# Performance work log

Measured on AMD Instinct MI355X. Metric: run time of the kernel, lower is better.

The kernel has to match this reference:

```python
import jax, jax.numpy as jnp
import numpy as np

IN_FEATURES = 256
N_HEADS = 4
N_HIDDEN = 128  # out_features, concat=False
SLOPE = 0.1
NEG_INF = -9e15


def setup_inputs() -> dict:
    key = jax.random.key(0)
    k1, k2, k3, k4 = jax.random.split(key, 4)
    N = 8192
    h = jax.random.normal(k1, (N, IN_FEATURES), dtype=jnp.float32)
    adj_mat = jax.random.randint(k2, (N, N), 0, 2, dtype=jnp.int32)
    # xavier_normal with gain=1.414
    std_W = 1.414 * (2.0 / (IN_FEATURES + N_HIDDEN * N_HEADS)) ** 0.5
    W = jax.random.normal(k3, (IN_FEATURES, N_HIDDEN * N_HEADS), dtype=jnp.float32) * std_W
    std_a = 1.414 * (2.0 / (2 * N_HIDDEN + 1)) ** 0.5
    a = jax.random.normal(k4, (N_HEADS, 2 * N_HIDDEN, 1), dtype=jnp.float32) * std_a
    return {"h": h, "adj_mat": adj_mat, "W": W, "a": a}


def reference(h, adj_mat, W, a):
    N = h.shape[0]
    # linear projection -> [H, N, d]
    ht = (h @ W).reshape(N, N_HEADS, N_HIDDEN).transpose(1, 0, 2)
    # dropout is identity (eval / p effectively 0), then LeakyReLU
    ht = jnp.where(ht >= 0, ht, SLOPE * ht)
    # additive attention scores: src[h,i] + tgt[h,j]
    src = jnp.einsum('hnd,hd->hn', ht, a[:, :N_HIDDEN, 0])  # [H, N]
    tgt = jnp.einsum('hnd,hd->hn', ht, a[:, N_HIDDEN:, 0])  # [H, N]
    e = src[:, :, None] + tgt[:, None, :]                   # [H, N, N]
    e = jnp.where(adj_mat[None, :, :] > 0, e, NEG_INF)
    attn = jax.nn.softmax(e, axis=-1)
    # weighted sum and mean over heads (concat=False)
    out = jnp.einsum('hnm,hmd->hnd', attn, ht).mean(axis=0)  # [N, d]
    return out
```

## Files before the change

kernel.cpp:

```cpp
#include <hip/hip_runtime.h>


typedef unsigned short u16;
typedef unsigned int u32;
using bf16x8 = __attribute__((ext_vector_type(8))) short;
using f32x4  = __attribute__((ext_vector_type(4))) float;

__device__ __forceinline__ u16 f2bf(float f) {
  u32 u = __float_as_uint(f);
  return (u16)((u + 0x7FFFu + ((u >> 16) & 1u)) >> 16);
}
__device__ __forceinline__ float bf2f(u16 u) {
  return __uint_as_float(((u32)u) << 16);
}

__global__ void transpose_w(const float* __restrict__ W, float* __restrict__ Wt) {
  __shared__ float tile[32][33];
  int cb = blockIdx.x * 32, kb = blockIdx.y * 32;
  int tc = threadIdx.x & 31, tr = threadIdx.x >> 5;
  for (int p = 0; p < 32; p += 8)
    tile[tr + p][tc] = W[(size_t)(kb + tr + p) * 512 + cb + tc];
  __syncthreads();
  for (int p = 0; p < 32; p += 8)
    Wt[(size_t)(cb + tr + p) * 256 + kb + tc] = tile[tc][tr + p];
}

__global__ void ht_gemm(const float* __restrict__ h, const float* __restrict__ Wt,
                        u16* __restrict__ HT) {
  __shared__ __align__(16) u16 Abuf[128 * 40];
  __shared__ __align__(16) u16 Bbuf[128 * 40];
  int tid = threadIdx.x;
  int cb = blockIdx.x, rb = blockIdx.y;
  int r0 = rb * 128, c0 = cb * 128;
  int lane = tid & 63, wv = tid >> 6;
  int wr = wv >> 1, wc = wv & 1;
  int mrow = lane & 15, q = lane >> 4;
  int ch = tid & 7, m0 = tid >> 3;

  f32x4 acc[4][4];
#pragma unroll
  for (int i = 0; i < 4; i++)
#pragma unroll
    for (int j = 0; j < 4; j++) acc[i][j] = f32x4{0.f, 0.f, 0.f, 0.f};

  for (int kt = 0; kt < 256; kt += 32) {
    __syncthreads();
#pragma unroll
    for (int mp = 0; mp < 128; mp += 32) {
      int m = m0 + mp;
      float4 v = *(const float4*)(&h[(size_t)(r0 + m) * 256 + kt + ch * 4]);
      uint2 p;
      p.x = (u32)f2bf(v.x) | ((u32)f2bf(v.y) << 16);
      p.y = (u32)f2bf(v.z) | ((u32)f2bf(v.w) << 16);
      *(uint2*)(&Abuf[m * 40 + ch * 4]) = p;
      float4 u = *(const float4*)(&Wt[(size_t)(c0 + m) * 256 + kt + ch * 4]);
      uint2 r;
      r.x = (u32)f2bf(u.x) | ((u32)f2bf(u.y) << 16);
      r.y = (u32)f2bf(u.z) | ((u32)f2bf(u.w) << 16);
      *(uint2*)(&Bbuf[m * 40 + ch * 4]) = r;
    }
    __syncthreads();
    bf16x8 af[4], bfv[4];
#pragma unroll
    for (int i = 0; i < 4; i++)
      af[i] = *(const bf16x8*)(&Abuf[(wr * 64 + i * 16 + mrow) * 40 + q * 8]);
#pragma unroll
    for (int j = 0; j < 4; j++)
      bfv[j] = *(const bf16x8*)(&Bbuf[(wc * 64 + j * 16 + mrow) * 40 + q * 8]);
#pragma unroll
    for (int i = 0; i < 4; i++)
#pragma unroll
      for (int j = 0; j < 4; j++)
        acc[i][j] = __builtin_amdgcn_mfma_f32_16x16x32_bf16(af[i], bfv[j], acc[i][j], 0, 0, 0);
  }
#pragma unroll
  for (int i = 0; i < 4; i++)
#pragma unroll
    for (int j = 0; j < 4; j++)
#pragma unroll
      for (int r = 0; r < 4; r++) {
        int gi = r0 + wr * 64 + i * 16 + q * 4 + r;
        int gc = c0 + wc * 64 + j * 16 + mrow;
        float v = acc[i][j][r];
        v = v >= 0.f ? v : 0.1f * v;
        HT[(size_t)gi * 512 + gc] = f2bf(v);
      }
}

__global__ void build_yt(const u16* __restrict__ HT, const float* __restrict__ a,
                         u16* __restrict__ Yt) {
  __shared__ u16 sht[64][528];
  __shared__ float swv[64 * 4];
  __shared__ float sa[512];
  int t = threadIdx.x;
  int j0 = blockIdx.x * 64;
  for (int i = t; i < 512; i += 256) {
    int g = i >> 7, d = i & 127;
    sa[i] = a[g * 256 + 128 + d];
  }
#pragma unroll
  for (int p = 0; p < 16; ++p) {
    int el = t + 256 * p;
    int row = el >> 6, col8 = el & 63;
    *(uint4*)(&sht[row][col8 * 8]) = *(const uint4*)(&HT[(size_t)(j0 + row) * 512 + col8 * 8]);
  }
  __syncthreads();
  {
    int jl = t >> 2, g = t & 3;
    float acc = 0.f;
#pragma unroll
    for (int d8 = 0; d8 < 16; ++d8) {
      bf16x8 v = *(const bf16x8*)(&sht[jl][g * 128 + d8 * 8]);
#pragma unroll
      for (int u = 0; u < 8; ++u)
        acc += bf2f((u16)v[u]) * sa[g * 128 + d8 * 8 + u];
    }
    swv[jl * 4 + g] = __expf(acc);
  }
  __syncthreads();
  int oj = (t & 7) * 8, oc = t >> 3;
  for (int pass = 0; pass < 17; ++pass) {
    int c = pass * 32 + oc;
    if (c >= 528) break;
    u32 pk[4] = {0u, 0u, 0u, 0u};
    if (c < 512) {
      int g = c >> 7;
#pragma unroll
      for (int u = 0; u < 4; ++u) {
        int j = oj + 2 * u;
        float v0 = bf2f(sht[j][c]) * swv[j * 4 + g];
        float v1 = bf2f(sht[j + 1][c]) * swv[(j + 1) * 4 + g];
        pk[u] = (u32)f2bf(v0) | ((u32)f2bf(v1) << 16);
      }
    } else if (c < 516) {
      int g = c - 512;
#pragma unroll
      for (int u = 0; u < 4; ++u) {
        int j = oj + 2 * u;
        float v0 = swv[j * 4 + g];
        float v1 = swv[(j + 1) * 4 + g];
        pk[u] = (u32)f2bf(v0) | ((u32)f2bf(v1) << 16);
      }
    }
    *(uint4*)(&Yt[(size_t)c * 8192 + j0 + oj]) = make_uint4(pk[0], pk[1], pk[2], pk[3]);
  }
}

__global__ __launch_bounds__(256, 2) void adj_gemm(const int* __restrict__ adj,
                                                   const u16* __restrict__ Yt,
                                                   float* __restrict__ C,
                                                   float* __restrict__ S) {
  __shared__ __align__(16) u16 Abuf[2][64 * 32];
  int tid = threadIdx.x;
  int rb = blockIdx.x, kh = blockIdx.y;
  int r0 = rb * 64, k0 = kh * 2048;
  int lane = tid & 63, wv = tid >> 6;
  int mrow = lane & 15, q = lane >> 4;
  int qs = q ^ ((mrow >> 1) & 3);
  int am = tid >> 2, aq = tid & 3;
  int asw = am * 32 + ((aq ^ ((am >> 1) & 3)) * 8);
  const int* aptr = &adj[(size_t)(r0 + am) * 8192 + k0 + aq * 8];
  const u16* bbase = &Yt[(size_t)(wv * 128 + mrow) * 8192 + k0 + q * 8];
  const u16* dbase = &Yt[(size_t)(512 + mrow) * 8192 + k0 + q * 8];

  f32x4 acc[4][8];
#pragma unroll
  for (int i = 0; i < 4; i++)
#pragma unroll
    for (int j = 0; j < 8; j++) acc[i][j] = f32x4{0.f, 0.f, 0.f, 0.f};
  f32x4 accD[4];
#pragma unroll
  for (int i = 0; i < 4; i++) accD[i] = f32x4{0.f, 0.f, 0.f, 0.f};

  {
    int4 v0 = *(const int4*)(aptr);
    int4 v1 = *(const int4*)(aptr + 4);
    uint4 pk;
    pk.x = 16256u * ((u32)v0.x | ((u32)v0.y << 16));
    pk.y = 16256u * ((u32)v0.z | ((u32)v0.w << 16));
    pk.z = 16256u * ((u32)v1.x | ((u32)v1.y << 16));
    pk.w = 16256u * ((u32)v1.z | ((u32)v1.w << 16));
    *(uint4*)(&Abuf[0][asw]) = pk;
  }
  asm volatile("s_waitcnt lgkmcnt(0)" ::: "memory");
  __builtin_amdgcn_s_barrier();

  for (int t = 0; t < 64; ++t) {
    int cur = t & 1;
    size_t koff = (size_t)t * 32;
    bf16x8 bfv[8];
#pragma unroll
    for (int j = 0; j < 8; j++)
      bfv[j] = *(const bf16x8*)(bbase + (size_t)j * 16 * 8192 + koff);
    bf16x8 bd;
    if (wv == 0) bd = *(const bf16x8*)(dbase + koff);
    int4 v0, v1;
    if (t < 63) {
      const int* ap = aptr + (size_t)(t + 1) * 32;
      v0 = *(const int4*)(ap);
      v1 = *(const int4*)(ap + 4);
    }
    bf16x8 af[4];
#pragma unroll
    for (int i = 0; i < 4; i++)
      af[i] = *(const bf16x8*)(&Abuf[cur][(i * 16 + mrow) * 32 + qs * 8]);
#pragma unroll
    for (int j = 0; j < 8; j++)
#pragma unroll
      for (int i = 0; i < 4; i++)
        acc[i][j] = __builtin_amdgcn_mfma_f32_16x16x32_bf16(af[i], bfv[j], acc[i][j], 0, 0, 0);
    if (wv == 0) {
#pragma unroll
      for (int i = 0; i < 4; i++)
        accD[i] = __builtin_amdgcn_mfma_f32_16x16x32_bf16(af[i], bd, accD[i], 0, 0, 0);
    }
    if (t < 63) {
      uint4 pk;
      pk.x = 16256u * ((u32)v0.x | ((u32)v0.y << 16));
      pk.y = 16256u * ((u32)v0.z | ((u32)v0.w << 16));
      pk.z = 16256u * ((u32)v1.x | ((u32)v1.y << 16));
      pk.w = 16256u * ((u32)v1.z | ((u32)v1.w << 16));
      *(uint4*)(&Abuf[cur ^ 1][asw]) = pk;
    }
    asm volatile("s_waitcnt lgkmcnt(0)" ::: "memory");
    __builtin_amdgcn_s_barrier();
  }

  float* Ck = C + (size_t)kh * 8192 * 512;
#pragma unroll
  for (int i = 0; i < 4; i++)
#pragma unroll
    for (int j = 0; j < 8; j++)
#pragma unroll
      for (int r = 0; r < 4; r++) {
        int gi = r0 + i * 16 + q * 4 + r;
        int gc = wv * 128 + j * 16 + mrow;
        Ck[(size_t)gi * 512 + gc] = acc[i][j][r];
      }
  if (wv == 0 && mrow < 4) {
    float* Sk = S + (size_t)kh * 4 * 8192;
#pragma unroll
    for (int i = 0; i < 4; i++)
#pragma unroll
      for (int r = 0; r < 4; r++) {
        int gi = r0 + i * 16 + q * 4 + r;
        Sk[(size_t)mrow * 8192 + gi] = accD[i][r];
      }
  }
}

__global__ void finalize_gat(const float* __restrict__ C, const float* __restrict__ S,
                             float* __restrict__ out) {
  int idx = blockIdx.x * 256 + threadIdx.x;
  int i = idx >> 7, d = idx & 127;
  float s = 0.f;
#pragma unroll
  for (int g = 0; g < 4; ++g) {
    float num = 0.f, den = 0.f;
#pragma unroll
    for (int kh = 0; kh < 4; ++kh) {
      num += C[(size_t)kh * 8192 * 512 + (size_t)i * 512 + g * 128 + d];
      den += S[(size_t)kh * 4 * 8192 + (size_t)g * 8192 + i];
    }
    s += num / den;
  }
  out[idx] = 0.25f * s;
}

extern "C" void kernel_launch(void* const* d_in, const int* in_sizes, int n_in,
                              void* d_out, int out_size, void* d_ws, size_t ws_size,
                              hipStream_t stream) {
  const float* h   = (const float*)d_in[0];
  const int*   adj = (const int*)d_in[1];
  const float* W   = (const float*)d_in[2];
  const float* a   = (const float*)d_in[3];
  float* out = (float*)d_out;
  char* ws = (char*)d_ws;
  float* Wt = (float*)(ws + 0);
  u16*   HT = (u16*)(ws + 524288);
  u16*   Yt = (u16*)(ws + 8912896);
  float* C  = (float*)(ws + 17563648);
  float* S  = (float*)(ws + 84672512);

  transpose_w<<<dim3(16, 8), 256, 0, stream>>>(W, Wt);
  ht_gemm<<<dim3(4, 64), 256, 0, stream>>>(h, Wt, HT);
  build_yt<<<dim3(128), 256, 0, stream>>>(HT, a, Yt);
  adj_gemm<<<dim3(128, 4), 256, 0, stream>>>(adj, Yt, C, S);
  finalize_gat<<<dim3(4096), 256, 0, stream>>>(C, S, out);
}
```

Before: 527.4 us.

## Stage 128-wide adjacency tiles per barrier and double-buffer B fragment loads

The adj_gemm main loop now stages a 64x128 adjacency tile (four 32-wide chunks in separate padded LDS slabs) per iteration instead of 64x32. This cuts the loop from 64 to 16 iterations and so reduces the number of barriers. Each thread now loads 128 contiguous bytes of adj per row instead of 32, which should make the global reads wider. Within an iteration, Yt fragment loads for the next k-chunk are issued while the MFMAs for the current chunk run, using two register sets. The cost is more registers (eight int4 prefetch values plus two B fragment sets) and more LDS, which may lower occupancy below the 2-blocks launch bound target.

```diff
diff --git a/kernel.cpp b/kernel.cpp
--- a/kernel.cpp
+++ b/kernel.cpp
@@ -150,16 +150,17 @@
                                                    const u16* __restrict__ Yt,
                                                    float* __restrict__ C,
                                                    float* __restrict__ S) {
-  __shared__ __align__(16) u16 Abuf[2][64 * 32];
+  __shared__ __align__(16) u16 Abuf[2][4][2080];
   int tid = threadIdx.x;
   int rb = blockIdx.x, kh = blockIdx.y;
   int r0 = rb * 64, k0 = kh * 2048;
   int lane = tid & 63, wv = tid >> 6;
   int mrow = lane & 15, q = lane >> 4;
   int qs = q ^ ((mrow >> 1) & 3);
-  int am = tid >> 2, aq = tid & 3;
-  int asw = am * 32 + ((aq ^ ((am >> 1) & 3)) * 8);
-  const int* aptr = &adj[(size_t)(r0 + am) * 8192 + k0 + aq * 8];
+  int ar = tid >> 2, akc = tid & 3;
+  int asw = ar * 32;
+  int arx = (ar >> 1) & 3;
+  const int* aptr = &adj[(size_t)(r0 + ar) * 8192 + k0 + akc * 32];
   const u16* bbase = &Yt[(size_t)(wv * 128 + mrow) * 8192 + k0 + q * 8];
   const u16* dbase = &Yt[(size_t)(512 + mrow) * 8192 + k0 + q * 8];
 
@@ -172,59 +173,92 @@
 #pragma unroll
   for (int i = 0; i < 4; i++) accD[i] = f32x4{0.f, 0.f, 0.f, 0.f};
 
+#define PACK_STORE(buf, V0, V1, S_)                                          \
+  {                                                                          \
+    uint4 pk;                                                                \
+    pk.x = 16256u * ((u32)V0.x | ((u32)V0.y << 16));                         \
+    pk.y = 16256u * ((u32)V0.z | ((u32)V0.w << 16));                         \
+    pk.z = 16256u * ((u32)V1.x | ((u32)V1.y << 16));                         \
+    pk.w = 16256u * ((u32)V1.z | ((u32)V1.w << 16));                         \
+    *(uint4*)(&Abuf[buf][akc][asw + ((S_) ^ arx) * 8]) = pk;                 \
+  }
+
   {
-    int4 v0 = *(const int4*)(aptr);
-    int4 v1 = *(const int4*)(aptr + 4);
-    uint4 pk;
-    pk.x = 16256u * ((u32)v0.x | ((u32)v0.y << 16));
-    pk.y = 16256u * ((u32)v0.z | ((u32)v0.w << 16));
-    pk.z = 16256u * ((u32)v1.x | ((u32)v1.y << 16));
-    pk.w = 16256u * ((u32)v1.z | ((u32)v1.w << 16));
-    *(uint4*)(&Abuf[0][asw]) = pk;
+    int4 w0 = *(const int4*)(aptr + 0);
+    int4 w1 = *(const int4*)(aptr + 4);
+    int4 w2 = *(const int4*)(aptr + 8);
+    int4 w3 = *(const int4*)(aptr + 12);
+    int4 w4 = *(const int4*)(aptr + 16);
+    int4 w5 = *(const int4*)(aptr + 20);
+    int4 w6 = *(const int4*)(aptr + 24);
+    int4 w7 = *(const int4*)(aptr + 28);
+    PACK_STORE(0, w0, w1, 0);
+    PACK_STORE(0, w2, w3, 1);
+    PACK_STORE(0, w4, w5, 2);
+    PACK_STORE(0, w6, w7, 3);
   }
   asm volatile("s_waitcnt lgkmcnt(0)" ::: "memory");
   __builtin_amdgcn_s_barrier();
 
-  for (int t = 0; t < 64; ++t) {
+#define LOADB(dst, dd, T_, KC_)                                              \
+  {                                                                          \
+    size_t o = (size_t)(T_)*128 + (KC_)*32;                                  \
+    _Pragma("unroll") for (int j = 0; j < 8; j++)                            \
+        dst[j] = *(const bf16x8*)(bbase + (size_t)j * 16 * 8192 + o);        \
+    if (wv == 0) dd = *(const bf16x8*)(dbase + o);                           \
+  }
+
+#define MFMA_CHUNK(bv, bd_, KC_)                                             \
+  {                                                                          \
+    bf16x8 af[4];                                                            \
+    _Pragma("unroll") for (int i = 0; i < 4; i++)                            \
+        af[i] = *(const bf16x8*)(&Abuf[cur][KC_][(i * 16 + mrow) * 32 + qs * 8]); \
+    _Pragma("unroll") for (int j = 0; j < 8; j++)                            \
+        _Pragma("unroll") for (int i = 0; i < 4; i++)                        \
+        acc[i][j] = __builtin_amdgcn_mfma_f32_16x16x32_bf16(af[i], bv[j], acc[i][j], 0, 0, 0); \
+    if (wv == 0) {                                                           \
+      _Pragma("unroll") for (int i = 0; i < 4; i++)                          \
+          accD[i] = __builtin_amdgcn_mfma_f32_16x16x32_bf16(af[i], bd_, accD[i], 0, 0, 0); \
+    }                                                                        \
+  }
+
+  for (int t = 0; t < 16; ++t) {
     int cur = t & 1;
-    size_t koff = (size_t)t * 32;
-    bf16x8 bfv[8];
-#pragma unroll
-    for (int j = 0; j < 8; j++)
-      bfv[j] = *(const bf16x8*)(bbase + (size_t)j * 16 * 8192 + koff);
-    bf16x8 bd;
-    if (wv == 0) bd = *(const bf16x8*)(dbase + koff);
-    int4 v0, v1;
-    if (t < 63) {
-      const int* ap = aptr + (size_t)(t + 1) * 32;
-      v0 = *(const int4*)(ap);
-      v1 = *(const int4*)(ap + 4);
-    }
-    bf16x8 af[4];
-#pragma unroll
-    for (int i = 0; i < 4; i++)
-      af[i] = *(const bf16x8*)(&Abuf[cur][(i * 16 + mrow) * 32 + qs * 8]);
-#pragma unroll
-    for (int j = 0; j < 8; j++)
-#pragma unroll
-      for (int i = 0; i < 4; i++)
-        acc[i][j] = __builtin_amdgcn_mfma_f32_16x16x32_bf16(af[i], bfv[j], acc[i][j], 0, 0, 0);
-    if (wv == 0) {
-#pragma unroll
-      for (int i = 0; i < 4; i++)
-        accD[i] = __builtin_amdgcn_mfma_f32_16x16x32_bf16(af[i], bd, accD[i], 0, 0, 0);
-    }
-    if (t < 63) {
-      uint4 pk;
-      pk.x = 16256u * ((u32)v0.x | ((u32)v0.y << 16));
-      pk.y = 16256u * ((u32)v0.z | ((u32)v0.w << 16));
-      pk.z = 16256u * ((u32)v1.x | ((u32)v1.y << 16));
-      pk.w = 16256u * ((u32)v1.z | ((u32)v1.w << 16));
-      *(uint4*)(&Abuf[cur ^ 1][asw]) = pk;
+    int4 w0, w1, w2, w3, w4, w5, w6, w7;
+    if (t < 15) {
+      const int* ap = aptr + (size_t)(t + 1) * 128;
+      w0 = *(const int4*)(ap + 0);
+      w1 = *(const int4*)(ap + 4);
+      w2 = *(const int4*)(ap + 8);
+      w3 = *(const int4*)(ap + 12);
+      w4 = *(const int4*)(ap + 16);
+      w5 = *(const int4*)(ap + 20);
+      w6 = *(const int4*)(ap + 24);
+      w7 = *(const int4*)(ap + 28);
+    }
+    bf16x8 bA[8], bB[8];
+    bf16x8 bdA, bdB;
+    LOADB(bA, bdA, t, 0);
+    LOADB(bB, bdB, t, 1);
+    MFMA_CHUNK(bA, bdA, 0);
+    LOADB(bA, bdA, t, 2);
+    MFMA_CHUNK(bB, bdB, 1);
+    LOADB(bB, bdB, t, 3);
+    MFMA_CHUNK(bA, bdA, 2);
+    MFMA_CHUNK(bB, bdB, 3);
+    if (t < 15) {
+      int nb = cur ^ 1;
+      PACK_STORE(nb, w0, w1, 0);
+      PACK_STORE(nb, w2, w3, 1);
+      PACK_STORE(nb, w4, w5, 2);
+      PACK_STORE(nb, w6, w7, 3);
     }
     asm volatile("s_waitcnt lgkmcnt(0)" ::: "memory");
     __builtin_amdgcn_s_barrier();
   }
+#undef LOADB
+#undef MFMA_CHUNK
+#undef PACK_STORE
 
   float* Ck = C + (size_t)kh * 8192 * 512;
 #pragma unroll
```

Result: slower. 584.3 us (+10.8%).

## Bit-pack adjacency tile into shared memory and expand via LUT per MFMA

Applied to the files above, without the earlier changes.

The adj_gemm kernel now loads the whole 64x2048 adjacency slice up front, compresses it to bitmasks with wave ballots into shared memory, and rebuilds bf16 A fragments from a 16-entry lookup table inside the main loop. This removes the per-iteration double-buffered LDS stores and the barrier from the K loop, so waves run the MFMA loop without synchronising. In exchange, the full adjacency load is serialized before any compute starts instead of overlapping with it, and each fragment now costs extra LDS lookups and bit manipulation.

```diff
diff --git a/kernel.cpp b/kernel.cpp
--- a/kernel.cpp
+++ b/kernel.cpp
@@ -3,6 +3,7 @@
 
 typedef unsigned short u16;
 typedef unsigned int u32;
+typedef unsigned long long u64;
 using bf16x8 = __attribute__((ext_vector_type(8))) short;
 using f32x4  = __attribute__((ext_vector_type(4))) float;
 
@@ -150,16 +151,29 @@
                                                    const u16* __restrict__ Yt,
                                                    float* __restrict__ C,
                                                    float* __restrict__ S) {
-  __shared__ __align__(16) u16 Abuf[2][64 * 32];
+  __shared__ u32 sA[64][65];
+  __shared__ u32 sLUT[16][2];
   int tid = threadIdx.x;
   int rb = blockIdx.x, kh = blockIdx.y;
   int r0 = rb * 64, k0 = kh * 2048;
   int lane = tid & 63, wv = tid >> 6;
   int mrow = lane & 15, q = lane >> 4;
-  int qs = q ^ ((mrow >> 1) & 3);
-  int am = tid >> 2, aq = tid & 3;
-  int asw = am * 32 + ((aq ^ ((am >> 1) & 3)) * 8);
-  const int* aptr = &adj[(size_t)(r0 + am) * 8192 + k0 + aq * 8];
+
+  if (tid < 16) {
+    u32 n = tid;
+    sLUT[n][0] = ((n & 1u) ? 0x3F80u : 0u) | ((n & 2u) ? 0x3F800000u : 0u);
+    sLUT[n][1] = ((n & 4u) ? 0x3F80u : 0u) | ((n & 8u) ? 0x3F800000u : 0u);
+  }
+
+#pragma unroll 8
+  for (int it = wv; it < 2048; it += 4) {
+    int row = it >> 5, u = it & 31;
+    int v = adj[(size_t)(r0 + row) * 8192 + k0 + u * 64 + lane];
+    u64 m = __ballot(v != 0);
+    if (!(lane & 31)) sA[row][u * 2 + (lane >> 5)] = (u32)(m >> lane);
+  }
+  __syncthreads();
+
   const u16* bbase = &Yt[(size_t)(wv * 128 + mrow) * 8192 + k0 + q * 8];
   const u16* dbase = &Yt[(size_t)(512 + mrow) * 8192 + k0 + q * 8];
 
@@ -172,38 +186,26 @@
 #pragma unroll
   for (int i = 0; i < 4; i++) accD[i] = f32x4{0.f, 0.f, 0.f, 0.f};
 
-  {
-    int4 v0 = *(const int4*)(aptr);
-    int4 v1 = *(const int4*)(aptr + 4);
-    uint4 pk;
-    pk.x = 16256u * ((u32)v0.x | ((u32)v0.y << 16));
-    pk.y = 16256u * ((u32)v0.z | ((u32)v0.w << 16));
-    pk.z = 16256u * ((u32)v1.x | ((u32)v1.y << 16));
-    pk.w = 16256u * ((u32)v1.z | ((u32)v1.w << 16));
-    *(uint4*)(&Abuf[0][asw]) = pk;
-  }
-  asm volatile("s_waitcnt lgkmcnt(0)" ::: "memory");
-  __builtin_amdgcn_s_barrier();
+  u32 sh = q * 8;
 
   for (int t = 0; t < 64; ++t) {
-    int cur = t & 1;
+    bf16x8 bfv[8];
     size_t koff = (size_t)t * 32;
-    bf16x8 bfv[8];
 #pragma unroll
     for (int j = 0; j < 8; j++)
       bfv[j] = *(const bf16x8*)(bbase + (size_t)j * 16 * 8192 + koff);
     bf16x8 bd;
     if (wv == 0) bd = *(const bf16x8*)(dbase + koff);
-    int4 v0, v1;
-    if (t < 63) {
-      const int* ap = aptr + (size_t)(t + 1) * 32;
-      v0 = *(const int4*)(ap);
-      v1 = *(const int4*)(ap + 4);
-    }
     bf16x8 af[4];
 #pragma unroll
-    for (int i = 0; i < 4; i++)
-      af[i] = *(const bf16x8*)(&Abuf[cur][(i * 16 + mrow) * 32 + qs * 8]);
+    for (int i = 0; i < 4; i++) {
+      u32 m = sA[i * 16 + mrow][t];
+      u32 b = (m >> sh) & 0xFFu;
+      u32 w[4];
+      *(uint2*)&w[0] = *(const uint2*)&sLUT[b & 15u][0];
+      *(uint2*)&w[2] = *(const uint2*)&sLUT[b >> 4][0];
+      af[i] = *(const bf16x8*)&w[0];
+    }
 #pragma unroll
     for (int j = 0; j < 8; j++)
 #pragma unroll
@@ -214,16 +216,6 @@
       for (int i = 0; i < 4; i++)
         accD[i] = __builtin_amdgcn_mfma_f32_16x16x32_bf16(af[i], bd, accD[i], 0, 0, 0);
     }
-    if (t < 63) {
-      uint4 pk;
-      pk.x = 16256u * ((u32)v0.x | ((u32)v0.y << 16));
-      pk.y = 16256u * ((u32)v0.z | ((u32)v0.w << 16));
-      pk.z = 16256u * ((u32)v1.x | ((u32)v1.y << 16));
-      pk.w = 16256u * ((u32)v1.z | ((u32)v1.w << 16));
-      *(uint4*)(&Abuf[cur ^ 1][asw]) = pk;
-    }
-    asm volatile("s_waitcnt lgkmcnt(0)" ::: "memory");
-    __builtin_amdgcn_s_barrier();
   }
 
   float* Ck = C + (size_t)kh * 8192 * 512;
```

Result: slower. 751.5 us (+42.5%).
